# Kernel tuning notes

Measured on AMD Instinct MI355X. Metric: run time of the kernel, lower is better.

Reference implementation:

```python
import jax, jax.numpy as jnp
import numpy as np

BOND = 64
RANK = 16
PATCH = 4
SIDE = 64          # num_patches_side = 256 // 4
OUT_C = 3
NODES = [1, 4, 16, 64, 256, 1024]   # per-layer node counts, depth=6
TOTAL_NODES = sum(NODES)            # 1365


def _norm_factor(key, shape):
    f = jax.random.normal(key, shape, dtype=jnp.float32)
    return f / (jnp.linalg.norm(f, axis=-1, keepdims=True) + 1e-8)


def setup_inputs() -> dict:
    key = jax.random.key(0)
    ks = jax.random.split(key, 10)
    B = 128
    x = jax.random.normal(ks[0], (B, 1, BOND), dtype=jnp.float32)
    # All layers' factors concatenated along the node axis (sliced per-layer).
    factor_in = _norm_factor(ks[1], (TOTAL_NODES, RANK, BOND))
    factor_tl = _norm_factor(ks[2], (TOTAL_NODES, RANK, BOND))
    factor_tr = _norm_factor(ks[3], (TOTAL_NODES, RANK, BOND))
    factor_bl = _norm_factor(ks[4], (TOTAL_NODES, RANK, BOND))
    factor_br = _norm_factor(ks[5], (TOTAL_NODES, RANK, BOND))
    scale = 1.0 + 0.02 * jax.random.normal(ks[6], (TOTAL_NODES, RANK), dtype=jnp.float32)
    head_w = jax.random.normal(ks[7], (OUT_C * PATCH * PATCH, BOND), dtype=jnp.float32) * (1.0 / np.sqrt(BOND))
    head_b = jnp.zeros((OUT_C * PATCH * PATCH,), dtype=jnp.float32)
    return {"x": x, "factor_in": factor_in, "factor_tl": factor_tl,
            "factor_tr": factor_tr, "factor_bl": factor_bl, "factor_br": factor_br,
            "scale": scale, "head_w": head_w, "head_b": head_b}


def _forward(x, factor_in, factor_tl, factor_tr, factor_bl, factor_br, scale, head_w, head_b):
    grid = 1
    off = 0
    for n in NODES:  # static loop over depth=6 layers
        fi = factor_in[off:off + n]
        sc = scale[off:off + n]
        lat = jnp.einsum('bni,nri->bnr', x, fi) * sc[None]        # [B,n,r]
        outs = jnp.stack(
            [jnp.einsum('bnr,nro->bno', lat, factor_tl[off:off + n]),
             jnp.einsum('bnr,nro->bno', lat, factor_tr[off:off + n]),
             jnp.einsum('bnr,nro->bno', lat, factor_bl[off:off + n]),
             jnp.einsum('bnr,nro->bno', lat, factor_br[off:off + n])],
            axis=2)                                               # [B,n,4,o]
        x4 = outs + x[:, :, None, :]
        # 'b (h w) (h2 w2) c -> b (h h2 w w2) c' with h=w=grid, h2=w2=2
        b, _, _, c = x4.shape
        x = x4.reshape(b, grid, grid, 2, 2, c).transpose(0, 1, 3, 2, 4, 5).reshape(b, 4 * n, c)
        grid *= 2
        off += n
    # head: Linear(bond -> c*p*p) then 'b (h w) (p1 p2 c) -> b c (h p1) (w p2)'
    y = x @ head_w.T + head_b                                     # [B, 4096, 48]
    b = y.shape[0]
    y = y.reshape(b, SIDE, SIDE, PATCH, PATCH, OUT_C)
    y = y.transpose(0, 5, 1, 3, 2, 4).reshape(b, OUT_C, SIDE * PATCH, SIDE * PATCH)
    return y


def reference(x, factor_in, factor_tl, factor_tr, factor_bl, factor_br, scale, head_w, head_b):
    return _forward(x, factor_in, factor_tl, factor_tr, factor_bl, factor_br, scale, head_w, head_b)
```

## Files before the change

### kernel.cpp

```cpp
#include <hip/hip_runtime.h>

constexpr int NTHR = 256;

typedef short  short8 __attribute__((ext_vector_type(8)));
typedef float  f32x4  __attribute__((ext_vector_type(4)));


__device__ __forceinline__ unsigned short f2bf(float f) {
    union { float f; unsigned u; } v; v.f = f;
    unsigned r = v.u + 0x7FFFu + ((v.u >> 16) & 1u);
    return (unsigned short)(r >> 16);
}

__device__ __forceinline__ void wlat(const float* __restrict__ f_in,
                                     const float* __restrict__ scale,
                                     int fo,
                                     const float (*xin)[64],
                                     float (*lat)[16],
                                     int lane)
{
    const int b = lane >> 5;
    const int r = (lane >> 1) & 15;
    const int h = lane & 1;
    const float4* fir = (const float4*)(f_in + (size_t)fo * 1024 + r * 64 + h * 32);
    const float4* xb  = (const float4*)(&xin[b][0] + h * 32);
    float p = 0.f;
#pragma unroll
    for (int i = 0; i < 8; ++i) {
        const float4 a = fir[i], c = xb[i];
        p += a.x * c.x + a.y * c.y + a.z * c.z + a.w * c.w;
    }
    p += __shfl_xor(p, 1);
    if (h == 0) lat[b][r] = p * scale[fo * 16 + r];
}

__device__ __forceinline__ void wchild(const float* __restrict__ fd,
                                       const float (*xin)[64],
                                       const float (*lat)[16],
                                       float (*xout)[64],
                                       int lane)
{
    const int o = lane;
    float f[16];
#pragma unroll
    for (int r = 0; r < 16; ++r) f[r] = fd[r * 64 + o];
#pragma unroll
    for (int b = 0; b < 2; ++b) {
        float acc = xin[b][o];
#pragma unroll
        for (int r = 0; r < 16; ++r) acc += lat[b][r] * f[r];
        xout[b][o] = acc;
    }
}

__device__ __forceinline__ void wchild_leaf(const float* __restrict__ fd,
                                            const float (*xin)[64],
                                            const float (*lat)[16],
                                            unsigned short* leaf,
                                            int nbase,
                                            int lane)
{
    const int o = lane;
    float f[16];
#pragma unroll
    for (int r = 0; r < 16; ++r) f[r] = fd[r * 64 + o];
#pragma unroll
    for (int b = 0; b < 2; ++b) {
        float acc = xin[b][o];
#pragma unroll
        for (int r = 0; r < 16; ++r) acc += lat[b][r] * f[r];
        leaf[(b * 8 + nbase) * 72 + o] = f2bf(acc);
    }
}

__global__ __launch_bounds__(NTHR, 3)
void qtree_kernel(const float* __restrict__ x,
                  const float* __restrict__ f_in,
                  const float* __restrict__ f_tl,
                  const float* __restrict__ f_tr,
                  const float* __restrict__ f_bl,
                  const float* __restrict__ f_br,
                  const float* __restrict__ scale,
                  const float* __restrict__ head_w,
                  const float* __restrict__ head_b,
                  float* __restrict__ out)
{
    __shared__ float s_xa[4][2][64];
    __shared__ float s_xb[4][2][64];
    __shared__ float s_x4[4][2][2][64];
    __shared__ float s_x5[4][4][2][64];
    __shared__ float s_lat[4][2][16];
    __shared__ unsigned short s_leaf[4][16][72];
    __shared__ float s_y[4][768];

    const int tid  = threadIdx.x;
    const int wv   = tid >> 6;
    const int lane = tid & 63;
    const int n    = lane & 15;
    const int q    = lane >> 4;
    const int n3   = blockIdx.x;
    const int bg   = blockIdx.y;
    const int jy   = blockIdx.z;
    const int y3   = n3 >> 3, x3 = n3 & 7;

    const float* fdir[4] = { f_tl, f_tr, f_bl, f_br };

    short8 afrag[3][2];
#pragma unroll
    for (int mt = 0; mt < 3; ++mt)
#pragma unroll
        for (int kc = 0; kc < 2; ++kc) {
            const float* src = head_w + (mt * 16 + n) * 64 + kc * 32 + q * 8;
            short8 a;
#pragma unroll
            for (int j = 0; j < 8; ++j) a[j] = (short)f2bf(src[j]);
            afrag[mt][kc] = a;
        }
    f32x4 accinit[3];
#pragma unroll
    for (int mt = 0; mt < 3; ++mt)
#pragma unroll
        for (int r = 0; r < 4; ++r) accinit[mt][r] = head_b[mt * 16 + q * 4 + r];
    const int lb = n >> 3, ldx = (n >> 2) & 1, lc = n & 3;
    const int lcy = lc >> 1, lcx = lc & 1;
    const int sy_base = lb * 384 + lcy * 64 + ldx * 8 + lcx * 4;
    int sy_ofs[3][4];
#pragma unroll
    for (int mt = 0; mt < 3; ++mt)
#pragma unroll
        for (int r = 0; r < 4; ++r) {
            const int o = mt * 16 + q * 4 + r;
            sy_ofs[mt][r] = sy_base + (o % 3) * 128 + (o / 12) * 16 + ((o / 3) & 3);
        }

    float (*xa)[64]  = s_xa[wv];
    float (*xb)[64]  = s_xb[wv];
    float (*lat)[16] = s_lat[wv];
    unsigned short* leaf = &s_leaf[wv][0][0];
    float* sy = s_y[wv];

#pragma unroll
    for (int b = 0; b < 2; ++b)
        xa[b][lane] = x[(size_t)(bg * 8 + wv * 2 + b) * 64 + lane];

    {
        wlat(f_in, scale, 0, xa, lat, lane);
        const int d = ((y3 >> 2) << 1) | (x3 >> 2);
        wchild(fdir[d], xa, lat, xb, lane);
    }
    {
        const int fo = 1 + ((y3 >> 2) * 2 + (x3 >> 2));
        wlat(f_in, scale, fo, xb, lat, lane);
        const int d = (((y3 >> 1) & 1) << 1) | ((x3 >> 1) & 1);
        wchild(fdir[d] + (size_t)fo * 1024, xb, lat, xa, lane);
    }
    {
        const int fo = 5 + ((y3 >> 1) * 4 + (x3 >> 1));
        wlat(f_in, scale, fo, xa, lat, lane);
        const int d = ((y3 & 1) << 1) | (x3 & 1);
        wchild(fdir[d] + (size_t)fo * 1024, xa, lat, xb, lane);
    }
    {
        const int fo = 21 + n3;
        wlat(f_in, scale, fo, xb, lat, lane);
#pragma unroll
        for (int jx = 0; jx < 2; ++jx)
            wchild(fdir[2 * jy + jx] + (size_t)fo * 1024, xb, lat, s_x4[wv][jx], lane);
    }

    for (int jx = 0; jx < 2; ++jx) {
        const int y4 = 2 * y3 + jy, x4c = 2 * x3 + jx;
        const int fo4 = 85 + y4 * 16 + x4c;
        wlat(f_in, scale, fo4, s_x4[wv][jx], lat, lane);
#pragma unroll
        for (int e = 0; e < 4; ++e)
            wchild(fdir[e] + (size_t)fo4 * 1024, s_x4[wv][jx], lat, s_x5[wv][e], lane);

        for (int p = 0; p < 2; ++p) {
#pragma unroll
            for (int dx2 = 0; dx2 < 2; ++dx2) {
                const int e = 2 * p + dx2;
                const int fo5 = 341 + (2 * y4 + p) * 32 + (2 * x4c + dx2);
                wlat(f_in, scale, fo5, s_x5[wv][e], lat, lane);
#pragma unroll
                for (int c = 0; c < 4; ++c)
                    wchild_leaf(fdir[c] + (size_t)fo5 * 1024, s_x5[wv][e], lat,
                                leaf, dx2 * 4 + c, lane);
            }

            f32x4 acc[3];
#pragma unroll
            for (int mt = 0; mt < 3; ++mt) acc[mt] = accinit[mt];
#pragma unroll
            for (int kc = 0; kc < 2; ++kc) {
                const short8 bfrag = *(const short8*)&s_leaf[wv][n][kc * 32 + q * 8];
#pragma unroll
                for (int mt = 0; mt < 3; ++mt)
                    acc[mt] = __builtin_amdgcn_mfma_f32_16x16x32_bf16(afrag[mt][kc], bfrag, acc[mt], 0, 0, 0);
            }

#pragma unroll
            for (int mt = 0; mt < 3; ++mt)
#pragma unroll
                for (int r = 0; r < 4; ++r) sy[sy_ofs[mt][r]] = acc[mt][r];

            const int base_row = (4 * y3 + 2 * jy + p) * 8;
            const int base_col = (4 * x3 + 2 * jx) * 8;
#pragma unroll
            for (int s = 0; s < 3; ++s) {
                const int i  = lane + 64 * s;
                const int c4 = i & 3;
                const int r2 = (i >> 2) & 7;
                const int bc = i >> 5;
                const float4 v = *(const float4*)&sy[(bc * 8 + r2) * 16 + c4 * 4];
                const size_t off = ((size_t)((bg * 8 + wv * 2 + bc / 3) * 3 + (bc % 3))) * 65536
                                 + (size_t)(base_row + r2) * 256 + base_col + c4 * 4;
                *(float4*)&out[off] = v;
            }
        }
    }
}

extern "C" void kernel_launch(void* const* d_in, const int* in_sizes, int n_in,
                              void* d_out, int out_size, void* d_ws, size_t ws_size,
                              hipStream_t stream) {
    const float* x    = (const float*)d_in[0];
    const float* f_in = (const float*)d_in[1];
    const float* f_tl = (const float*)d_in[2];
    const float* f_tr = (const float*)d_in[3];
    const float* f_bl = (const float*)d_in[4];
    const float* f_br = (const float*)d_in[5];
    const float* sc   = (const float*)d_in[6];
    const float* hw   = (const float*)d_in[7];
    const float* hb   = (const float*)d_in[8];
    float* out = (float*)d_out;

    dim3 grid(64, 16, 2);
    qtree_kernel<<<grid, NTHR, 0, stream>>>(x, f_in, f_tl, f_tr, f_bl, f_br, sc, hw, hb, out);
}
```

Measured before the change: 318.5 us.

## Alias per-wave LDS buffers and pack offsets to raise occupancy

Replaces the separate per-wave shared arrays with one aliased pool, so leaf, head output and the level-5 buffers share storage and LDS per block shrinks. Level-5 children are now computed per row (p) on demand, which cuts x5 storage. Head bias moves to LDS and the scatter offsets are packed two per register, lowering register pressure so the launch bound can request 8 blocks per CU instead of 3. The risk is spills from the tighter register target, plus the recomputation cost of splitting the child computation across p iterations.

```diff
diff --git a/kernel.cpp b/kernel.cpp
--- a/kernel.cpp
+++ b/kernel.cpp
@@ -73,7 +73,7 @@
     }
 }
 
-__global__ __launch_bounds__(NTHR, 3)
+__global__ __launch_bounds__(NTHR, 8)
 void qtree_kernel(const float* __restrict__ x,
                   const float* __restrict__ f_in,
                   const float* __restrict__ f_tl,
@@ -85,13 +85,8 @@
                   const float* __restrict__ head_b,
                   float* __restrict__ out)
 {
-    __shared__ float s_xa[4][2][64];
-    __shared__ float s_xb[4][2][64];
-    __shared__ float s_x4[4][2][2][64];
-    __shared__ float s_x5[4][4][2][64];
-    __shared__ float s_lat[4][2][16];
-    __shared__ unsigned short s_leaf[4][16][72];
-    __shared__ float s_y[4][768];
+    __shared__ __align__(16) float s_pool[4][1152];
+    __shared__ float s_hb[48];
 
     const int tid  = threadIdx.x;
     const int wv   = tid >> 6;
@@ -105,6 +100,18 @@
 
     const float* fdir[4] = { f_tl, f_tr, f_bl, f_br };
 
+    float* P = s_pool[wv];
+    float (*xa)[64]  = (float(*)[64])P;
+    float (*xb)[64]  = (float(*)[64])(P + 128);
+    unsigned short* leaf = (unsigned short*)P;
+    float (*x5)[64]  = (float(*)[64])(P + 576);
+    float* sy        = P;
+    float (*x4)[64]  = (float(*)[64])(P + 832);
+    float (*lat)[16] = (float(*)[16])(P + 1088);
+    float (*lat4)[16]= (float(*)[16])(P + 1120);
+
+    if (lane < 48) s_hb[lane] = head_b[lane];
+
     short8 afrag[3][2];
 #pragma unroll
     for (int mt = 0; mt < 3; ++mt)
@@ -116,28 +123,22 @@
             for (int j = 0; j < 8; ++j) a[j] = (short)f2bf(src[j]);
             afrag[mt][kc] = a;
         }
-    f32x4 accinit[3];
-#pragma unroll
-    for (int mt = 0; mt < 3; ++mt)
-#pragma unroll
-        for (int r = 0; r < 4; ++r) accinit[mt][r] = head_b[mt * 16 + q * 4 + r];
+
     const int lb = n >> 3, ldx = (n >> 2) & 1, lc = n & 3;
     const int lcy = lc >> 1, lcx = lc & 1;
     const int sy_base = lb * 384 + lcy * 64 + ldx * 8 + lcx * 4;
-    int sy_ofs[3][4];
-#pragma unroll
-    for (int mt = 0; mt < 3; ++mt)
-#pragma unroll
-        for (int r = 0; r < 4; ++r) {
-            const int o = mt * 16 + q * 4 + r;
-            sy_ofs[mt][r] = sy_base + (o % 3) * 128 + (o / 12) * 16 + ((o / 3) & 3);
+    unsigned sy_pk[6];
+#pragma unroll
+    for (int i = 0; i < 6; ++i) {
+        unsigned lohi[2];
+#pragma unroll
+        for (int j = 0; j < 2; ++j) {
+            const int t = 2 * i + j;
+            const int o = (t >> 2) * 16 + q * 4 + (t & 3);
+            lohi[j] = (unsigned)(sy_base + (o % 3) * 128 + (o / 12) * 16 + ((o / 3) & 3));
         }
-
-    float (*xa)[64]  = s_xa[wv];
-    float (*xb)[64]  = s_xb[wv];
-    float (*lat)[16] = s_lat[wv];
-    unsigned short* leaf = &s_leaf[wv][0][0];
-    float* sy = s_y[wv];
+        sy_pk[i] = lohi[0] | (lohi[1] << 16);
+    }
 
 #pragma unroll
     for (int b = 0; b < 2; ++b)
@@ -165,35 +166,36 @@
         wlat(f_in, scale, fo, xb, lat, lane);
 #pragma unroll
         for (int jx = 0; jx < 2; ++jx)
-            wchild(fdir[2 * jy + jx] + (size_t)fo * 1024, xb, lat, s_x4[wv][jx], lane);
+            wchild(fdir[2 * jy + jx] + (size_t)fo * 1024, xb, lat, &x4[2 * jx], lane);
     }
 
     for (int jx = 0; jx < 2; ++jx) {
         const int y4 = 2 * y3 + jy, x4c = 2 * x3 + jx;
         const int fo4 = 85 + y4 * 16 + x4c;
-        wlat(f_in, scale, fo4, s_x4[wv][jx], lat, lane);
-#pragma unroll
-        for (int e = 0; e < 4; ++e)
-            wchild(fdir[e] + (size_t)fo4 * 1024, s_x4[wv][jx], lat, s_x5[wv][e], lane);
+        wlat(f_in, scale, fo4, &x4[2 * jx], lat4, lane);
 
         for (int p = 0; p < 2; ++p) {
 #pragma unroll
+            for (int dx2 = 0; dx2 < 2; ++dx2)
+                wchild(fdir[2 * p + dx2] + (size_t)fo4 * 1024, &x4[2 * jx], lat4,
+                       &x5[2 * dx2], lane);
+#pragma unroll
             for (int dx2 = 0; dx2 < 2; ++dx2) {
-                const int e = 2 * p + dx2;
                 const int fo5 = 341 + (2 * y4 + p) * 32 + (2 * x4c + dx2);
-                wlat(f_in, scale, fo5, s_x5[wv][e], lat, lane);
+                wlat(f_in, scale, fo5, &x5[2 * dx2], lat, lane);
 #pragma unroll
                 for (int c = 0; c < 4; ++c)
-                    wchild_leaf(fdir[c] + (size_t)fo5 * 1024, s_x5[wv][e], lat,
+                    wchild_leaf(fdir[c] + (size_t)fo5 * 1024, &x5[2 * dx2], lat,
                                 leaf, dx2 * 4 + c, lane);
             }
 
             f32x4 acc[3];
 #pragma unroll
-            for (int mt = 0; mt < 3; ++mt) acc[mt] = accinit[mt];
+            for (int mt = 0; mt < 3; ++mt)
+                acc[mt] = *(const f32x4*)&s_hb[mt * 16 + q * 4];
 #pragma unroll
             for (int kc = 0; kc < 2; ++kc) {
-                const short8 bfrag = *(const short8*)&s_leaf[wv][n][kc * 32 + q * 8];
+                const short8 bfrag = *(const short8*)&leaf[n * 72 + kc * 32 + q * 8];
 #pragma unroll
                 for (int mt = 0; mt < 3; ++mt)
                     acc[mt] = __builtin_amdgcn_mfma_f32_16x16x32_bf16(afrag[mt][kc], bfrag, acc[mt], 0, 0, 0);
@@ -202,7 +204,11 @@
 #pragma unroll
             for (int mt = 0; mt < 3; ++mt)
 #pragma unroll
-                for (int r = 0; r < 4; ++r) sy[sy_ofs[mt][r]] = acc[mt][r];
+                for (int r = 0; r < 4; ++r) {
+                    const int t = mt * 4 + r;
+                    const int ofs = (sy_pk[t >> 1] >> (16 * (t & 1))) & 0xffff;
+                    sy[ofs] = acc[mt][r];
+                }
 
             const int base_row = (4 * y3 + 2 * jy + p) * 8;
             const int base_col = (4 * x3 + 2 * jx) * 8;
```

Result: slower. 449.2 us (+41.0%).
